# Performance work log

Hardware: AMD Instinct MI355X
Metric: run time of the kernel (lower is better)

Reference implementation:

```python
import jax, jax.numpy as jnp
import numpy as np

B, S, D, H = 2, 4096, 256, 8
P = 64               # proj_dim_l
R = S // P           # proj_dim_r = 64, P*R == S
DH = D // H          # head_dim = 32


def setup_inputs() -> dict:
    key = jax.random.key(0)
    kx, kl, kr, kv, ko = jax.random.split(key, 5)
    scale = 0.05  # stand-in for xavier-uniform scale
    x  = jax.random.normal(kx, (B, S, D), dtype=jnp.float32)
    Wl = jax.random.normal(kl, (D, P), dtype=jnp.float32) * scale
    Wr = jax.random.normal(kr, (D, R), dtype=jnp.float32) * scale
    Wv = jax.random.normal(kv, (D, D), dtype=jnp.float32) * scale
    Wo = jax.random.normal(ko, (D, D), dtype=jnp.float32) * scale
    return {"x": x, "Wl": Wl, "Wr": Wr, "Wv": Wv, "Wo": Wo}


def reference(x, Wl, Wr, Wv, Wo):
    b, s, d = x.shape
    # value projection + head split -> (b, H, S, DH). Dropout p=0 (eval) = identity.
    v = (x @ Wv).reshape(b, s, H, DH).transpose(0, 2, 1, 3)
    # factorized score: row n is vec(outer(l_n, r_n)) of length P*R == S
    l = x @ Wl                                   # (b, S, P)
    r = x @ Wr                                   # (b, S, R)
    attn = (l[:, :, :, None] * r[:, :, None, :]).reshape(b, s, s)  # (b, S, S)
    score = jax.nn.softmax(attn, axis=-1)        # (b, S, S)
    # shared score across heads, per-head value matmul
    o = jnp.einsum('bnm,bhmd->bhnd', score, v)   # (b, H, S, DH)
    o = o.transpose(0, 2, 1, 3).reshape(b, s, d) # concat heads
    return o @ Wo
```

## Files before the change

### kernel.cpp

```cpp
#include <hip/hip_runtime.h>
#include <hip/hip_bf16.h>

typedef __attribute__((ext_vector_type(8))) __bf16 bf16x8;
typedef __attribute__((ext_vector_type(4))) __bf16 bf16x4;
typedef __attribute__((ext_vector_type(4))) float  f32x4;

#define MFMA16(a, b, c) __builtin_amdgcn_mfma_f32_16x16x32_bf16((a), (b), (c), 0, 0, 0)

static constexpr size_t OFF_WVT  = 0;
static constexpr size_t OFF_WLT  = OFF_WVT + 256 * 256 * 2;
static constexpr size_t OFF_WRT  = OFF_WLT + 64 * 256 * 2;
static constexpr size_t OFF_VT   = 1u << 20;
static constexpr size_t OFF_L    = 6u << 20;
static constexpr size_t OFF_R    = 8u << 20;
static constexpr size_t OFF_PART = 10u << 20;
static constexpr size_t OFF_ZP   = 26u << 20;

__device__ __forceinline__ float fast_exp2(float x) {
  float e;
  asm("v_exp_f32 %0, %1" : "=v"(e) : "v"(x));
  return e;
}

__device__ __forceinline__ bf16x8 cvt8(float4 a, float4 b) {
  bf16x8 o;
  o[0] = (__bf16)a.x; o[1] = (__bf16)a.y; o[2] = (__bf16)a.z; o[3] = (__bf16)a.w;
  o[4] = (__bf16)b.x; o[5] = (__bf16)b.y; o[6] = (__bf16)b.z; o[7] = (__bf16)b.w;
  return o;
}

__device__ __forceinline__ void gll16(const __bf16* g, __bf16* l) {
  __builtin_amdgcn_global_load_lds((const __attribute__((address_space(1))) void*)g,
                                   (__attribute__((address_space(3))) void*)l,
                                   16, 0, 0);
}

__global__ __launch_bounds__(1024) void k_prepw(const float* __restrict__ Wv,
                                                const float* __restrict__ Wl,
                                                const float* __restrict__ Wr,
                                                const float* __restrict__ Wo,
                                                __bf16* __restrict__ Wvt,
                                                __bf16* __restrict__ Wlt,
                                                __bf16* __restrict__ Wrt) {
  __shared__ float red[3][256];
  const int blk = blockIdx.x;
  const int t = threadIdx.x;
  if (blk < 32) {
    const int idx = blk * 1024 + t;
    if (idx < 16384) {
      const int k = idx >> 6, n = idx & 63;
      Wlt[n * 256 + k] = (__bf16)Wl[idx];
    } else {
      const int j = idx - 16384;
      const int k = j >> 6, n = j & 63;
      Wrt[n * 256 + k] = (__bf16)Wr[j];
    }
  } else {
    const int k  = blk - 32;
    const int n  = t & 255;
    const int jq = t >> 8;
    const float* wvr = Wv + (size_t)k * 256 + jq * 64;
    const float* wor = Wo + (size_t)(jq * 64) * 256 + n;
    float a0 = 0.f, a1 = 0.f, a2 = 0.f, a3 = 0.f;
#pragma unroll 4
    for (int j = 0; j < 64; j += 4) {
      a0 += wvr[j + 0] * wor[(size_t)(j + 0) * 256];
      a1 += wvr[j + 1] * wor[(size_t)(j + 1) * 256];
      a2 += wvr[j + 2] * wor[(size_t)(j + 2) * 256];
      a3 += wvr[j + 3] * wor[(size_t)(j + 3) * 256];
    }
    const float s = (a0 + a1) + (a2 + a3);
    if (jq > 0) red[jq - 1][n] = s;
    __syncthreads();
    if (jq == 0)
      Wvt[(size_t)n * 256 + k] = (__bf16)(s + red[0][n] + red[1][n] + red[2][n]);
  }
}

__global__ __launch_bounds__(256) void k_proj(const float* __restrict__ x,
                                              const __bf16* __restrict__ Wvt,
                                              const __bf16* __restrict__ Wlt,
                                              const __bf16* __restrict__ Wrt,
                                              __bf16* __restrict__ Vt,
                                              float* __restrict__ lbuf,
                                              float* __restrict__ rbuf) {
  __shared__ __align__(16) char smem[16896];
  const int t = threadIdx.x;
  const int lane = t & 63, wave = t >> 6;
  const int l16 = lane & 15, quad = lane >> 4;
  const int wr = wave >> 1, wc = wave & 1;
  const int bid = blockIdx.x;
  const int q   = bid / 48;
  const int rmd = bid - q * 48;
  const int ct  = rmd >> 3;
  const int rbk = q * 8 + (rmd & 7);
  const __bf16* Wt;
  int colbase;
  if (ct < 4)       { Wt = Wvt; colbase = ct * 64; }
  else if (ct == 4) { Wt = Wlt; colbase = 0; }
  else              { Wt = Wrt; colbase = 0; }
  const int row0 = rbk * 64 + wr * 32;
  const int c0   = colbase + wc * 32;
  f32x4 acc[2][2] = {};
  for (int kk = 0; kk < 256; kk += 32) {
    const int ko = kk + quad * 8;
    const float* xr0 = x + (size_t)(row0 + l16) * 256 + ko;
    const float* xr1 = x + (size_t)(row0 + 16 + l16) * 256 + ko;
    bf16x8 a0 = cvt8(*(const float4*)xr0, *(const float4*)(xr0 + 4));
    bf16x8 a1 = cvt8(*(const float4*)xr1, *(const float4*)(xr1 + 4));
    bf16x8 b0 = *(const bf16x8*)(Wt + (size_t)(c0 + l16) * 256 + ko);
    bf16x8 b1 = *(const bf16x8*)(Wt + (size_t)(c0 + 16 + l16) * 256 + ko);
    acc[0][0] = MFMA16(a0, b0, acc[0][0]);
    acc[0][1] = MFMA16(a0, b1, acc[0][1]);
    acc[1][0] = MFMA16(a1, b0, acc[1][0]);
    acc[1][1] = MFMA16(a1, b1, acc[1][1]);
  }
  if (ct < 4) {
    __bf16* vs = (__bf16*)smem;
#pragma unroll
    for (int mt = 0; mt < 2; ++mt)
#pragma unroll
      for (int nt = 0; nt < 2; ++nt) {
        const int m8 = wr * 4 + mt * 2 + (quad >> 1);
        const int d  = wc * 32 + nt * 16 + l16;
        bf16x4 o;
        o.x = (__bf16)acc[mt][nt][0];
        o.y = (__bf16)acc[mt][nt][1];
        o.z = (__bf16)acc[mt][nt][2];
        o.w = (__bf16)acc[mt][nt][3];
        *(bf16x4*)(&vs[m8 * 512 + d * 8 + (quad & 1) * 4]) = o;
      }
    __syncthreads();
    const int m8 = t >> 5, s32 = t & 31;
    const int bat = rbk >> 6, mc = rbk & 63;
    bf16x8 a = *(const bf16x8*)(&vs[m8 * 512 + s32 * 16]);
    bf16x8 b = *(const bf16x8*)(&vs[m8 * 512 + s32 * 16 + 8]);
    __bf16* dst = Vt + (size_t)bat * 1048576 + (size_t)mc * 16384 +
                  m8 * 2048 + ct * 512 + s32 * 16;
    *(bf16x8*)dst       = a;
    *(bf16x8*)(dst + 8) = b;
  } else {
    float* lsf = (float*)smem;
#pragma unroll
    for (int mt = 0; mt < 2; ++mt)
#pragma unroll
      for (int nt = 0; nt < 2; ++nt) {
        const int col = wc * 32 + nt * 16 + l16;
        const int r0  = wr * 32 + mt * 16 + quad * 4;
#pragma unroll
        for (int rr = 0; rr < 4; ++rr)
          lsf[(r0 + rr) * 65 + col] = acc[mt][nt][rr];
      }
    __syncthreads();
    float* dstb = (ct == 4) ? lbuf : rbuf;
    const int row = t >> 2, cs = (t & 3) * 16;
    const float* src = lsf + row * 65 + cs;
    float* d = dstb + (size_t)(rbk * 64 + row) * 64 + cs;
#pragma unroll
    for (int v = 0; v < 4; ++v) {
      f32x4 o;
      o[0] = src[v * 4 + 0]; o[1] = src[v * 4 + 1];
      o[2] = src[v * 4 + 2]; o[3] = src[v * 4 + 3];
      *(f32x4*)(d + v * 4) = o;
    }
  }
}

__global__ __launch_bounds__(256, 2) void k_attn(const float* __restrict__ lbuf,
                                                 const float* __restrict__ rbuf,
                                                 const __bf16* __restrict__ Vt,
                                                 __bf16* __restrict__ part,
                                                 float* __restrict__ zpart) {
  __shared__ __align__(16) char smem[69888];
  __bf16* vb0 = (__bf16*)smem;
  __bf16* vb1 = (__bf16*)(smem + 16384);
  __bf16* vb2 = (__bf16*)(smem + 32768);
  __bf16* vb3 = (__bf16*)(smem + 49152);
  float*  ls  = (float*)(smem + 65536);
  const int t = threadIdx.x;
  const int lane = t & 63, w = t >> 6;
  const int l16 = lane & 15, quad = lane >> 4;
  const int wr = w >> 1, wc = w & 1;
  const int bid = blockIdx.x;
  const int cmb = bid & 7;
  const int sp  = cmb >> 1;
  const int bat = cmb & 1;
  const int rbl = bid >> 3;
  const int g0  = bat * 4096 + rbl * 64;
  const __bf16* Vbase = Vt + (size_t)bat * 1048576;
  const int ck0 = sp * 32;

  {
    const int row = t >> 2, c = (t & 3) * 4;
    f32x4 v = *(const f32x4*)(lbuf + (size_t)(g0 + row) * 64 + sp * 16 + c);
    ls[row * 17 + c + 0] = v[0];
    ls[row * 17 + c + 1] = v[1];
    ls[row * 17 + c + 2] = v[2];
    ls[row * 17 + c + 3] = v[3];
  }
  const float LOG2E = 1.44269504088896f;
  float rreg[2][16];
#pragma unroll
  for (int mt = 0; mt < 2; ++mt) {
    const float* rp = rbuf + (size_t)(g0 + wr * 32 + mt * 16 + l16) * 64;
    f32x4 a = *(const f32x4*)(rp + quad * 8);
    f32x4 b = *(const f32x4*)(rp + quad * 8 + 4);
    f32x4 c = *(const f32x4*)(rp + 32 + quad * 8);
    f32x4 d = *(const f32x4*)(rp + 32 + quad * 8 + 4);
#pragma unroll
    for (int j = 0; j < 4; ++j) {
      rreg[mt][j]      = a[j] * LOG2E;
      rreg[mt][4 + j]  = b[j] * LOG2E;
      rreg[mt][8 + j]  = c[j] * LOG2E;
      rreg[mt][12 + j] = d[j] * LOG2E;
    }
  }

  f32x4 acc[2][8] = {};
  float zacc[2][2] = {{0.f, 0.f}, {0.f, 0.f}};

#define STAGE(KC, DST)                                                          \
  {                                                                             \
    const __bf16* src = Vbase + (size_t)(ck0 + (KC)) * 8192;                    \
    _Pragma("unroll")                                                           \
    for (int i = 0; i < 4; ++i)                                                 \
      gll16(src + (size_t)(i * 256 + t) * 8, (DST) + (i * 256 + (w << 6)) * 8); \
  }

#define AF_COMPUTE(KC)                                                        \
  {                                                                           \
    const int c16 = (KC) >> 1, hf = ((KC) & 1) * 8;                           \
    _Pragma("unroll")                                                         \
    for (int mt = 0; mt < 2; ++mt) {                                          \
      const float lv = ls[(wr * 32 + mt * 16 + l16) * 17 + c16];              \
      _Pragma("unroll")                                                       \
      for (int j = 0; j < 8; ++j) {                                           \
        const float e = fast_exp2(lv * rreg[mt][hf + j]);                     \
        zacc[mt][(KC) & 1] += e;                                              \
        af[mt][j] = (__bf16)e;                                                \
      }                                                                       \
    }                                                                         \
  }

#define MFMA_PHASE(CUR)                                                       \
  {                                                                           \
    _Pragma("unroll")                                                         \
    for (int nt = 0; nt < 8; ++nt) {                                          \
      bf16x8 bv = *(const bf16x8*)((CUR) + quad * 2048 +                      \
                                   (wc * 128 + nt * 16 + l16) * 8);           \
      acc[0][nt] = MFMA16(af[0], bv, acc[0][nt]);                             \
      acc[1][nt] = MFMA16(af[1], bv, acc[1][nt]);                             \
    }                                                                         \
  }

#define STEP(CC, BCUR, SC, BST, VM)                                           \
  {                                                                           \
    STAGE(SC, BST);                                                           \
    bf16x8 af[2];                                                             \
    AF_COMPUTE(CC);                                                           \
    asm volatile("s_waitcnt vmcnt(" #VM ")" ::: "memory");                    \
    __builtin_amdgcn_s_barrier();                                             \
    __builtin_amdgcn_sched_barrier(0);                                        \
    MFMA_PHASE(BCUR);                                                         \
    __builtin_amdgcn_s_barrier();                                             \
    __builtin_amdgcn_sched_barrier(0);                                        \
  }

#define STEPX(CC, BCUR, VM)                                                   \
  {                                                                           \
    bf16x8 af[2];                                                             \
    AF_COMPUTE(CC);                                                           \
    asm volatile("s_waitcnt vmcnt(" #VM ")" ::: "memory");                    \
    __builtin_amdgcn_s_barrier();                                             \
    __builtin_amdgcn_sched_barrier(0);                                        \
    MFMA_PHASE(BCUR);                                                         \
    __builtin_amdgcn_s_barrier();                                             \
    __builtin_amdgcn_sched_barrier(0);                                        \
  }

  STAGE(0, vb0);
  STAGE(1, vb1);
  STAGE(2, vb2);
  __syncthreads();

  for (int c = 0; c < 28; c += 4) {
    STEP(c + 0, vb0, c + 3, vb3, 12);
    STEP(c + 1, vb1, c + 4, vb0, 12);
    STEP(c + 2, vb2, c + 5, vb1, 12);
    STEP(c + 3, vb3, c + 6, vb2, 12);
  }
  STEP (28, vb0, 31, vb3, 12);
  STEPX(29, vb1, 8);
  STEPX(30, vb2, 4);
  STEPX(31, vb3, 0);

#undef STAGE
#undef AF_COMPUTE
#undef MFMA_PHASE
#undef STEP
#undef STEPX

#pragma unroll
  for (int mt = 0; mt < 2; ++mt) {
    float z = zacc[mt][0] + zacc[mt][1];
    z += __shfl_xor(z, 16);
    z += __shfl_xor(z, 32);
    if (wc == 0 && quad == 0)
      zpart[(size_t)sp * 8192 + g0 + wr * 32 + mt * 16 + l16] = z;
  }

  __syncthreads();
  __bf16* ctile = (__bf16*)smem;
#pragma unroll
  for (int mt = 0; mt < 2; ++mt)
#pragma unroll
    for (int nt = 0; nt < 8; ++nt) {
      const int r0 = wr * 32 + mt * 16 + quad * 4;
      const int c  = wc * 128 + nt * 16 + l16;
#pragma unroll
      for (int rr = 0; rr < 4; ++rr)
        ctile[(r0 + rr) * 264 + c] = (__bf16)acc[mt][nt][rr];
    }
  __syncthreads();
  __bf16* pb = part + (size_t)sp * (8192 * 256);
#pragma unroll
  for (int p = 0; p < 8; ++p) {
    const int u = p * 256 + t;
    const int row = u >> 5, seg = u & 31;
    *(bf16x8*)(pb + (size_t)(g0 + row) * 256 + seg * 8) =
        *(const bf16x8*)(ctile + row * 264 + seg * 8);
  }
}

__global__ __launch_bounds__(256) void k_fix(const __bf16* __restrict__ part,
                                             const float* __restrict__ zpart,
                                             float* __restrict__ out) {
  const int idx = blockIdx.x * 256 + threadIdx.x;
  const int g = idx >> 5, seg = idx & 31;
  float z = 0.f;
#pragma unroll
  for (int s = 0; s < 4; ++s) z += zpart[(size_t)s * 8192 + g];
  const float iz = 1.0f / z;
  float sum[8] = {};
#pragma unroll
  for (int s = 0; s < 4; ++s) {
    bf16x8 p = *(const bf16x8*)(part + (size_t)s * (8192 * 256) + (size_t)g * 256 + seg * 8);
#pragma unroll
    for (int j = 0; j < 8; ++j) sum[j] += (float)p[j];
  }
  f32x4 o0, o1;
#pragma unroll
  for (int j = 0; j < 4; ++j) { o0[j] = sum[j] * iz; o1[j] = sum[4 + j] * iz; }
  float* dst = out + (size_t)g * 256 + seg * 8;
  *(f32x4*)dst       = o0;
  *(f32x4*)(dst + 4) = o1;
}

extern "C" void kernel_launch(void* const* d_in, const int* in_sizes, int n_in,
                              void* d_out, int out_size, void* d_ws, size_t ws_size,
                              hipStream_t stream) {
  const float* x  = (const float*)d_in[0];
  const float* Wl = (const float*)d_in[1];
  const float* Wr = (const float*)d_in[2];
  const float* Wv = (const float*)d_in[3];
  const float* Wo = (const float*)d_in[4];
  char* ws = (char*)d_ws;
  __bf16* Wvt = (__bf16*)(ws + OFF_WVT);
  __bf16* Wlt = (__bf16*)(ws + OFF_WLT);
  __bf16* Wrt = (__bf16*)(ws + OFF_WRT);
  __bf16* Vt  = (__bf16*)(ws + OFF_VT);
  float*  lb  = (float*)(ws + OFF_L);
  float*  rbf = (float*)(ws + OFF_R);
  __bf16* prt = (__bf16*)(ws + OFF_PART);
  float*  zp  = (float*)(ws + OFF_ZP);
  float*  out = (float*)d_out;

  k_prepw<<<288, 1024, 0, stream>>>(Wv, Wl, Wr, Wo, Wvt, Wlt, Wrt);
  k_proj<<<768, 256, 0, stream>>>(x, Wvt, Wlt, Wrt, Vt, lb, rbf);
  k_attn<<<512, 256, 0, stream>>>(lb, rbf, Vt, prt, zp);
  k_fix<<<1024, 256, 0, stream>>>(prt, zp, out);
}
```

Baseline: 121.8 us.

## Replace split-K attention and reduction kernel with column-split fused normalization

```diff
diff --git a/kernel.cpp b/kernel.cpp
--- a/kernel.cpp
+++ b/kernel.cpp
@@ -13,8 +13,6 @@
 static constexpr size_t OFF_VT   = 1u << 20;
 static constexpr size_t OFF_L    = 6u << 20;
 static constexpr size_t OFF_R    = 8u << 20;
-static constexpr size_t OFF_PART = 10u << 20;
-static constexpr size_t OFF_ZP   = 26u << 20;
 
 __device__ __forceinline__ float fast_exp2(float x) {
   float e;
@@ -169,34 +167,36 @@
 __global__ __launch_bounds__(256, 2) void k_attn(const float* __restrict__ lbuf,
                                                  const float* __restrict__ rbuf,
                                                  const __bf16* __restrict__ Vt,
-                                                 __bf16* __restrict__ part,
-                                                 float* __restrict__ zpart) {
-  __shared__ __align__(16) char smem[69888];
+                                                 float* __restrict__ out) {
+  __shared__ __align__(16) char smem[49664];
   __bf16* vb0 = (__bf16*)smem;
-  __bf16* vb1 = (__bf16*)(smem + 16384);
-  __bf16* vb2 = (__bf16*)(smem + 32768);
-  __bf16* vb3 = (__bf16*)(smem + 49152);
-  float*  ls  = (float*)(smem + 65536);
+  __bf16* vb1 = (__bf16*)(smem + 8192);
+  __bf16* vb2 = (__bf16*)(smem + 16384);
+  __bf16* vb3 = (__bf16*)(smem + 24576);
+  float*  ls  = (float*)(smem + 32768);
+  float*  zls = (float*)(smem + 49408);
   const int t = threadIdx.x;
   const int lane = t & 63, w = t >> 6;
   const int l16 = lane & 15, quad = lane >> 4;
   const int wr = w >> 1, wc = w & 1;
   const int bid = blockIdx.x;
-  const int cmb = bid & 7;
-  const int sp  = cmb >> 1;
-  const int bat = cmb & 1;
-  const int rbl = bid >> 3;
+  const int bat = bid & 1;
+  const int ch  = (bid >> 1) & 1;
+  const int rbl = bid >> 2;
   const int g0  = bat * 4096 + rbl * 64;
   const __bf16* Vbase = Vt + (size_t)bat * 1048576;
-  const int ck0 = sp * 32;
 
   {
-    const int row = t >> 2, c = (t & 3) * 4;
-    f32x4 v = *(const f32x4*)(lbuf + (size_t)(g0 + row) * 64 + sp * 16 + c);
-    ls[row * 17 + c + 0] = v[0];
-    ls[row * 17 + c + 1] = v[1];
-    ls[row * 17 + c + 2] = v[2];
-    ls[row * 17 + c + 3] = v[3];
+    const int row = t >> 2, c = (t & 3) * 16;
+    const float* lp = lbuf + (size_t)(g0 + row) * 64 + c;
+#pragma unroll
+    for (int v = 0; v < 4; ++v) {
+      f32x4 x4 = *(const f32x4*)(lp + v * 4);
+      ls[row * 65 + c + v * 4 + 0] = x4[0];
+      ls[row * 65 + c + v * 4 + 1] = x4[1];
+      ls[row * 65 + c + v * 4 + 2] = x4[2];
+      ls[row * 65 + c + v * 4 + 3] = x4[3];
+    }
   }
   const float LOG2E = 1.44269504088896f;
   float rreg[2][16];
@@ -216,15 +216,18 @@
     }
   }
 
-  f32x4 acc[2][8] = {};
+  f32x4 acc[2][4] = {};
   float zacc[2][2] = {{0.f, 0.f}, {0.f, 0.f}};
 
-#define STAGE(KC, DST)                                                          \
-  {                                                                             \
-    const __bf16* src = Vbase + (size_t)(ck0 + (KC)) * 8192;                    \
-    _Pragma("unroll")                                                           \
-    for (int i = 0; i < 4; ++i)                                                 \
-      gll16(src + (size_t)(i * 256 + t) * 8, (DST) + (i * 256 + (w << 6)) * 8); \
+#define STAGE(KC, DST)                                                        \
+  {                                                                           \
+    const __bf16* src = Vbase + (size_t)(KC) * 8192 + ch * 1024;              \
+    _Pragma("unroll")                                                         \
+    for (int i = 0; i < 2; ++i) {                                             \
+      const int unit = i * 256 + t;                                           \
+      gll16(src + (size_t)(unit >> 7) * 2048 + (unit & 127) * 8,              \
+            (DST) + (i * 256 + (w << 6)) * 8);                                \
+    }                                                                         \
   }
 
 #define AF_COMPUTE(KC)                                                        \
@@ -232,7 +235,7 @@
     const int c16 = (KC) >> 1, hf = ((KC) & 1) * 8;                           \
     _Pragma("unroll")                                                         \
     for (int mt = 0; mt < 2; ++mt) {                                          \
-      const float lv = ls[(wr * 32 + mt * 16 + l16) * 17 + c16];              \
+      const float lv = ls[(wr * 32 + mt * 16 + l16) * 65 + c16];              \
       _Pragma("unroll")                                                       \
       for (int j = 0; j < 8; ++j) {                                           \
         const float e = fast_exp2(lv * rreg[mt][hf + j]);                     \
@@ -245,9 +248,9 @@
 #define MFMA_PHASE(CUR)                                                       \
   {                                                                           \
     _Pragma("unroll")                                                         \
-    for (int nt = 0; nt < 8; ++nt) {                                          \
-      bf16x8 bv = *(const bf16x8*)((CUR) + quad * 2048 +                      \
-                                   (wc * 128 + nt * 16 + l16) * 8);           \
+    for (int nt = 0; nt < 4; ++nt) {                                          \
+      bf16x8 bv = *(const bf16x8*)((CUR) + quad * 1024 +                      \
+                                   (wc * 64 + nt * 16 + l16) * 8);            \
       acc[0][nt] = MFMA16(af[0], bv, acc[0][nt]);                             \
       acc[1][nt] = MFMA16(af[1], bv, acc[1][nt]);                             \
     }                                                                         \
@@ -283,16 +286,16 @@
   STAGE(2, vb2);
   __syncthreads();
 
-  for (int c = 0; c < 28; c += 4) {
-    STEP(c + 0, vb0, c + 3, vb3, 12);
-    STEP(c + 1, vb1, c + 4, vb0, 12);
-    STEP(c + 2, vb2, c + 5, vb1, 12);
-    STEP(c + 3, vb3, c + 6, vb2, 12);
-  }
-  STEP (28, vb0, 31, vb3, 12);
-  STEPX(29, vb1, 8);
-  STEPX(30, vb2, 4);
-  STEPX(31, vb3, 0);
+  for (int c = 0; c < 124; c += 4) {
+    STEP(c + 0, vb0, c + 3, vb3, 6);
+    STEP(c + 1, vb1, c + 4, vb0, 6);
+    STEP(c + 2, vb2, c + 5, vb1, 6);
+    STEP(c + 3, vb3, c + 6, vb2, 6);
+  }
+  STEP (124, vb0, 127, vb3, 6);
+  STEPX(125, vb1, 4);
+  STEPX(126, vb2, 2);
+  STEPX(127, vb3, 0);
 
 #undef STAGE
 #undef AF_COMPUTE
@@ -306,54 +309,33 @@
     z += __shfl_xor(z, 16);
     z += __shfl_xor(z, 32);
     if (wc == 0 && quad == 0)
-      zpart[(size_t)sp * 8192 + g0 + wr * 32 + mt * 16 + l16] = z;
+      zls[wr * 32 + mt * 16 + l16] = 1.0f / z;
   }
 
   __syncthreads();
-  __bf16* ctile = (__bf16*)smem;
+  float* ctile = (float*)smem;
 #pragma unroll
   for (int mt = 0; mt < 2; ++mt)
 #pragma unroll
-    for (int nt = 0; nt < 8; ++nt) {
+    for (int nt = 0; nt < 4; ++nt) {
       const int r0 = wr * 32 + mt * 16 + quad * 4;
-      const int c  = wc * 128 + nt * 16 + l16;
+      const int cl = wc * 64 + nt * 16 + l16;
 #pragma unroll
       for (int rr = 0; rr < 4; ++rr)
-        ctile[(r0 + rr) * 264 + c] = (__bf16)acc[mt][nt][rr];
+        ctile[(r0 + rr) * 132 + cl] = acc[mt][nt][rr];
     }
   __syncthreads();
-  __bf16* pb = part + (size_t)sp * (8192 * 256);
+  float* pb = out + (size_t)g0 * 256 + ch * 128;
 #pragma unroll
   for (int p = 0; p < 8; ++p) {
     const int u = p * 256 + t;
     const int row = u >> 5, seg = u & 31;
-    *(bf16x8*)(pb + (size_t)(g0 + row) * 256 + seg * 8) =
-        *(const bf16x8*)(ctile + row * 264 + seg * 8);
-  }
-}
-
-__global__ __launch_bounds__(256) void k_fix(const __bf16* __restrict__ part,
-                                             const float* __restrict__ zpart,
-                                             float* __restrict__ out) {
-  const int idx = blockIdx.x * 256 + threadIdx.x;
-  const int g = idx >> 5, seg = idx & 31;
-  float z = 0.f;
-#pragma unroll
-  for (int s = 0; s < 4; ++s) z += zpart[(size_t)s * 8192 + g];
-  const float iz = 1.0f / z;
-  float sum[8] = {};
-#pragma unroll
-  for (int s = 0; s < 4; ++s) {
-    bf16x8 p = *(const bf16x8*)(part + (size_t)s * (8192 * 256) + (size_t)g * 256 + seg * 8);
-#pragma unroll
-    for (int j = 0; j < 8; ++j) sum[j] += (float)p[j];
-  }
-  f32x4 o0, o1;
-#pragma unroll
-  for (int j = 0; j < 4; ++j) { o0[j] = sum[j] * iz; o1[j] = sum[4 + j] * iz; }
-  float* dst = out + (size_t)g * 256 + seg * 8;
-  *(f32x4*)dst       = o0;
-  *(f32x4*)(dst + 4) = o1;
+    const float iz = zls[row];
+    f32x4 v = *(const f32x4*)(ctile + row * 132 + seg * 4);
+    f32x4 o;
+    o[0] = v[0] * iz; o[1] = v[1] * iz; o[2] = v[2] * iz; o[3] = v[3] * iz;
+    *(f32x4*)(pb + (size_t)row * 256 + seg * 4) = o;
+  }
 }
 
 extern "C" void kernel_launch(void* const* d_in, const int* in_sizes, int n_in,
@@ -371,12 +353,9 @@
   __bf16* Vt  = (__bf16*)(ws + OFF_VT);
   float*  lb  = (float*)(ws + OFF_L);
   float*  rbf = (float*)(ws + OFF_R);
-  __bf16* prt = (__bf16*)(ws + OFF_PART);
-  float*  zp  = (float*)(ws + OFF_ZP);
   float*  out = (float*)d_out;
 
   k_prepw<<<288, 1024, 0, stream>>>(Wv, Wl, Wr, Wo, Wvt, Wlt, Wrt);
   k_proj<<<768, 256, 0, stream>>>(x, Wvt, Wlt, Wrt, Vt, lb, rbf);
-  k_attn<<<512, 256, 0, stream>>>(lb, rbf, Vt, prt, zp);
-  k_fix<<<1024, 256, 0, stream>>>(prt, zp, out);
-}
+  k_attn<<<256, 256, 0, stream>>>(lb, rbf, Vt, out);
+}
```

After: 138.2 us. 1.13x slower.
